# Kernel tuning notes

Measured on AMD Instinct MI355X. Metric: run time of the kernel, lower is better.

Reference implementation:

```python
import jax, jax.numpy as jnp
import numpy as np
from jax.scipy.special import logsumexp

EPS = 0.05        # entropic regularization (blur^p)
N_ITERS = 20      # Sinkhorn iterations
N, M, D = 8192, 8192, 64


def setup_inputs() -> dict:
    key = jax.random.key(0)
    k1, k2, k3, k4 = jax.random.split(key, 4)
    return {
        "a": jax.random.uniform(k1, (N,), dtype=jnp.float32),
        "x": jax.random.normal(k2, (N, D), dtype=jnp.float32),
        "b": jax.random.uniform(k3, (M,), dtype=jnp.float32),
        "y": jax.random.normal(k4, (M, D), dtype=jnp.float32),
    }


def reference(a, x, b, y):
    eps = EPS
    # _normalize_weights: probability simplex
    a = a / jnp.sum(a)
    b = b / jnp.sum(b)
    loga = jnp.log(a)
    logb = jnp.log(b)
    # squared-Euclidean cost C_ij = ||x_i - y_j||^2, built via one GEMM (online kernel's math)
    x2 = jnp.sum(x * x, axis=1)            # [N]
    y2 = jnp.sum(y * y, axis=1)            # [M]
    C = x2[:, None] + y2[None, :] - 2.0 * (x @ y.T)   # [N, M]

    # log-domain Sinkhorn: f_i = -eps * LSE_j( log b_j + (g_j - C_ij)/eps )
    def softmin_rows(g_, C_, logw):   # reduce over columns j -> [N]
        return -eps * logsumexp(logw[None, :] + (g_[None, :] - C_) / eps, axis=1)

    def softmin_cols(f_, C_, logw):   # reduce over rows i -> [M]
        return -eps * logsumexp(logw[:, None] + (f_[:, None] - C_) / eps, axis=0)

    def body(i, fg):
        f_, g_ = fg
        f_ = softmin_rows(g_, C, logb)
        g_ = softmin_cols(f_, C, loga)
        return (f_, g_)

    f0 = jnp.zeros_like(a)
    g0 = jnp.zeros_like(b)
    f, g = jax.lax.fori_loop(0, N_ITERS, body, (f0, g0))

    # GeomLoss-style: one final symmetric update from detached potentials (Danskin)
    f_d = jax.lax.stop_gradient(f)
    g_d = jax.lax.stop_gradient(g)
    f_fin = softmin_rows(g_d, C, logb)
    g_fin = softmin_cols(f_d, C, loga)
    # OT_eps(a, b) = <a, f> + <b, g>
    return jnp.sum(a * f_fin) + jnp.sum(b * g_fin)
```

## Files before the change

### kernel.cpp

```cpp
#include <hip/hip_runtime.h>
#include <hip/hip_bf16.h>

#define EPS       0.05f
#define N_ITERS   20
#define NR        8192
#define DIM       64
#define LOG2E     1.4426950408889634f
#define LN2       0.6931471805599453f
#define S2        (2.0f * LOG2E / EPS)
#define EPSLN2    (EPS * LN2)
#define NEGINF    (-1e30f)

typedef __attribute__((ext_vector_type(8))) short short8;
typedef __attribute__((ext_vector_type(4))) float float4v;

__device__ __forceinline__ float wave_reduce_sum(float v) {
    #pragma unroll
    for (int m = 1; m < 64; m <<= 1) v += __shfl_xor(v, m, 64);
    return v;
}

__device__ __forceinline__ float merge_l(float m0, float s0, float m1, float s1) {
    float M = fmaxf(m0, m1);
    float S = s0 * __builtin_amdgcn_exp2f(m0 - M) + s1 * __builtin_amdgcn_exp2f(m1 - M);
    return M + __builtin_amdgcn_logf(S);
}

__global__ void sums_kernel(const float* __restrict__ a, const float* __restrict__ b,
                            float* __restrict__ sums) {
    __shared__ float red[32];
    int tid = threadIdx.x;
    float pa = 0.f, pb = 0.f;
    for (int i = tid; i < NR; i += blockDim.x) { pa += a[i]; pb += b[i]; }
    pa = wave_reduce_sum(pa);
    pb = wave_reduce_sum(pb);
    int wid = tid >> 6, ln = tid & 63;
    if (ln == 0) { red[wid] = pa; red[wid + 16] = pb; }
    __syncthreads();
    if (tid == 0) {
        float sa = 0.f, sb = 0.f;
        int nw = blockDim.x >> 6;
        for (int w = 0; w < nw; w++) { sa += red[w]; sb += red[w + 16]; }
        sums[0] = logf(sa); sums[1] = logf(sb); sums[2] = sa; sums[3] = sb;
    }
}

__global__ void prep_kernel(const float* __restrict__ x, const float* __restrict__ y,
                            const float* __restrict__ a, const float* __restrict__ b,
                            const float* __restrict__ sums,
                            short8* __restrict__ xr, short8* __restrict__ yr,
                            short8* __restrict__ xs, short8* __restrict__ ys,
                            float* __restrict__ x2, float* __restrict__ y2,
                            float* __restrict__ la2, float* __restrict__ lb2,
                            float2* __restrict__ Pb) {
    int gid = blockIdx.x * 256 + threadIdx.x;
    bool isx = gid < NR * 8;
    int cid = isx ? gid : gid - NR * 8;
    int row = cid >> 3;
    int c   = cid & 7;
    const float4* src = (const float4*)(isx ? x : y);
    float4 v0 = src[row * 16 + c * 2];
    float4 v1 = src[row * 16 + c * 2 + 1];

    short8 st;
    st[0] = __bfloat16_as_short(__float2bfloat16(v0.x));
    st[1] = __bfloat16_as_short(__float2bfloat16(v0.y));
    st[2] = __bfloat16_as_short(__float2bfloat16(v0.z));
    st[3] = __bfloat16_as_short(__float2bfloat16(v0.w));
    st[4] = __bfloat16_as_short(__float2bfloat16(v1.x));
    st[5] = __bfloat16_as_short(__float2bfloat16(v1.y));
    st[6] = __bfloat16_as_short(__float2bfloat16(v1.z));
    st[7] = __bfloat16_as_short(__float2bfloat16(v1.w));

    (isx ? xr : yr)[row * 8 + c] = st;
    int T = row >> 4, ln = row & 15, f = c >> 2, q = c & 3;
    (isx ? xs : ys)[T * 128 + f * 64 + q * 16 + ln] = st;

    float sq = v0.x*v0.x + v0.y*v0.y + v0.z*v0.z + v0.w*v0.w
             + v1.x*v1.x + v1.y*v1.y + v1.z*v1.z + v1.w*v1.w;
    #pragma unroll
    for (int m = 1; m < 8; m <<= 1) sq += __shfl_xor(sq, m, 64);

    if (c == 0) {
        if (isx) {
            x2[row] = sq;
            la2[row] = (logf(a[row]) - sums[0]) * LOG2E;
        } else {
            y2[row] = sq;
            lb2[row] = (logf(b[row]) - sums[1]) * LOG2E;
            Pb[row]      = make_float2(sq * (LOG2E / EPS), 1.0f);
            Pb[NR + row] = make_float2(NEGINF, 0.0f);
        }
    }
}

#define LSE4(acc, c4, mm, ss)                                            \
    {                                                                    \
        float z0 = fmaf(S2, (acc)[0], (c4).x);                           \
        float z1 = fmaf(S2, (acc)[1], (c4).y);                           \
        float z2 = fmaf(S2, (acc)[2], (c4).z);                           \
        float z3 = fmaf(S2, (acc)[3], (c4).w);                           \
        float zm = fmaxf(fmaxf(z0, z1), fmaxf(z2, z3));                  \
        float mn = fmaxf((mm), zm);                                      \
        float e  = __builtin_amdgcn_exp2f((mm) - mn);                    \
        float p  = (__builtin_amdgcn_exp2f(z0 - mn)                      \
                  + __builtin_amdgcn_exp2f(z1 - mn))                     \
                 + (__builtin_amdgcn_exp2f(z2 - mn)                      \
                  + __builtin_amdgcn_exp2f(z3 - mn));                    \
        (ss) = fmaf((ss), e, p);                                         \
        (mm) = mn;                                                       \
    }

__global__ __launch_bounds__(1024, 4) void pass_kernel(
        const short8* __restrict__ matXr,
        const short8* __restrict__ matYs,
        const float2* __restrict__ Pin,
        const float* __restrict__ lw2col,
        float2* __restrict__ Pout) {
    __shared__ __attribute__((aligned(16))) float cbl[4096];
    __shared__ float2 comb[64][16];

    const int tid = threadIdx.x;
    const int bi  = blockIdx.x;
    const int h   = bi & 1;
    const int rb  = (bi >> 1) * 64;
    const int cb0 = h * 4096;

    {
        int j = cb0 + tid * 4;
        const float4* P0 = (const float4*)(Pin + j);
        const float4* P1 = (const float4*)(Pin + NR + j);
        float4 q0 = P0[0], q1 = P0[1];
        float4 r0 = P1[0], r1 = P1[1];
        float4 lw = *(const float4*)(lw2col + j);
        float4 cb;
        cb.x = lw.x - merge_l(q0.x, q0.y, r0.x, r0.y);
        cb.y = lw.y - merge_l(q0.z, q0.w, r0.z, r0.w);
        cb.z = lw.z - merge_l(q1.x, q1.y, r1.x, r1.y);
        cb.w = lw.w - merge_l(q1.z, q1.w, r1.z, r1.w);
        *(float4*)(cbl + tid * 4) = cb;
    }

    const int w    = tid >> 6;
    const int lane = tid & 63;
    const int quad = lane >> 4;
    const int ln   = lane & 15;

    short8 xf0[4], xf1[4];
    #pragma unroll
    for (int t = 0; t < 4; t++) {
        xf0[t] = matXr[(rb + t * 16 + ln) * 8 + quad];
        xf1[t] = matXr[(rb + t * 16 + ln) * 8 + quad + 4];
    }

    const int T0 = h * 256 + w * 16;
    const short8* yp = matYs + (size_t)T0 * 128 + lane;

    float m[4], s[4];
    #pragma unroll
    for (int t = 0; t < 4; t++) { m[t] = NEGINF; s[t] = 0.f; }

    __syncthreads();

    #pragma unroll 2
    for (int jt = 0; jt < 16; jt++) {
        short8 ya0 = yp[0];
        short8 ya1 = yp[64];
        float4 c4  = *(const float4*)(cbl + (w * 16 + jt) * 16 + quad * 4);
        yp += 128;

        float4v acc[4];
        #pragma unroll
        for (int t = 0; t < 4; t++) {
            float4v z = {0.f, 0.f, 0.f, 0.f};
            z = __builtin_amdgcn_mfma_f32_16x16x32_bf16(ya0, xf0[t], z, 0, 0, 0);
            z = __builtin_amdgcn_mfma_f32_16x16x32_bf16(ya1, xf1[t], z, 0, 0, 0);
            acc[t] = z;
        }
        #pragma unroll
        for (int t = 0; t < 4; t++) LSE4(acc[t], c4, m[t], s[t]);
    }

    #pragma unroll
    for (int mask = 16; mask < 64; mask <<= 1) {
        #pragma unroll
        for (int t = 0; t < 4; t++) {
            float mo = __shfl_xor(m[t], mask, 64);
            float so = __shfl_xor(s[t], mask, 64);
            float M  = fmaxf(m[t], mo);
            s[t] = s[t] * __builtin_amdgcn_exp2f(m[t] - M)
                 + so   * __builtin_amdgcn_exp2f(mo   - M);
            m[t] = M;
        }
    }

    if (lane < 16) {
        #pragma unroll
        for (int t = 0; t < 4; t++)
            comb[t * 16 + ln][w] = make_float2(m[t], s[t]);
    }
    __syncthreads();

    if (tid < 64) {
        float2 c = comb[tid][0];
        float M = c.x, S = c.y;
        #pragma unroll
        for (int cc = 1; cc < 16; cc++) {
            float2 p = comb[tid][cc];
            float Mn = fmaxf(M, p.x);
            S = S * __builtin_amdgcn_exp2f(M - Mn)
              + p.y * __builtin_amdgcn_exp2f(p.x - Mn);
            M = Mn;
        }
        Pout[h * NR + rb + tid] = make_float2(M, S);
    }
}

__global__ void reduce_kernel(const float* __restrict__ a, const float* __restrict__ b,
                              const float* __restrict__ sums,
                              const float* __restrict__ x2, const float* __restrict__ y2,
                              const float2* __restrict__ Pff, const float2* __restrict__ Pgf,
                              float* __restrict__ out) {
    __shared__ float red[32];
    int tid = threadIdx.x;
    float da = 0.f, db = 0.f;
    for (int i = tid; i < NR; i += blockDim.x) {
        float2 f0 = Pff[i], f1 = Pff[NR + i];
        float2 g0 = Pgf[i], g1 = Pgf[NR + i];
        float fv = x2[i] - EPSLN2 * merge_l(f0.x, f0.y, f1.x, f1.y);
        float gv = y2[i] - EPSLN2 * merge_l(g0.x, g0.y, g1.x, g1.y);
        da += a[i] * fv;
        db += b[i] * gv;
    }
    da = wave_reduce_sum(da);
    db = wave_reduce_sum(db);
    int wid = tid >> 6, ln = tid & 63;
    if (ln == 0) { red[wid] = da; red[wid + 16] = db; }
    __syncthreads();
    if (tid == 0) {
        float DA = 0.f, DB = 0.f;
        int nw = blockDim.x >> 6;
        for (int w = 0; w < nw; w++) { DA += red[w]; DB += red[w + 16]; }
        out[0] = DA / sums[2] + DB / sums[3];
    }
}

extern "C" void kernel_launch(void* const* d_in, const int* in_sizes, int n_in,
                              void* d_out, int out_size, void* d_ws, size_t ws_size,
                              hipStream_t stream) {
    const float* a = (const float*)d_in[0];
    const float* x = (const float*)d_in[1];
    const float* b = (const float*)d_in[2];
    const float* y = (const float*)d_in[3];

    char* ws = (char*)d_ws;
    short8* xr = (short8*)ws;
    short8* yr = (short8*)(ws + (1 << 20));
    short8* xs = (short8*)(ws + (2 << 20));
    short8* ys = (short8*)(ws + (3 << 20));
    float* fp  = (float*)(ws + (4 << 20));
    float* x2  = fp;
    float* y2  = fp + NR;
    float* la2 = fp + 2 * NR;
    float* lb2 = fp + 3 * NR;
    float2* P   = (float2*)(fp + 4 * NR);
    float2* Pf  = P;
    float2* Pb  = P + 2 * NR;
    float2* Pff = P + 4 * NR;
    float2* Pgf = P + 6 * NR;
    float* sums = (float*)(P + 8 * NR);

    sums_kernel<<<1, 1024, 0, stream>>>(a, b, sums);
    prep_kernel<<<(2 * NR * 8) / 256, 256, 0, stream>>>(x, y, a, b, sums,
                                                        xr, yr, xs, ys,
                                                        x2, y2, la2, lb2, Pb);

    for (int it = 0; it < N_ITERS; it++) {
        pass_kernel<<<256, 1024, 0, stream>>>(xr, ys, Pb, lb2, Pf);
        pass_kernel<<<256, 1024, 0, stream>>>(yr, xs, Pf, la2, Pb);
    }
    pass_kernel<<<256, 1024, 0, stream>>>(xr, ys, Pb, lb2, Pff);
    pass_kernel<<<256, 1024, 0, stream>>>(yr, xs, Pf, la2, Pgf);

    reduce_kernel<<<1, 1024, 0, stream>>>(a, b, sums, x2, y2, Pff, Pgf, (float*)d_out);
}
```

Before: 924.4 us.

## Split columns into four partitions with 128-row blocks per workgroup

Each pass block now covers 128 rows and a quarter of the columns, instead of 64 rows and half the columns. Two groups of eight waves share each 16-column strip, so the Y fragments and column constants are reused across twice as many rows. Each block reads and writes four partial log-sum-exp buffers instead of two, so the consumer merges four partials. Grid size stays at 256 blocks. The price is a larger partial-merge step in each pass and in the final reduction.

```diff
diff --git a/kernel.cpp b/kernel.cpp
--- a/kernel.cpp
+++ b/kernel.cpp
@@ -10,6 +10,7 @@
 #define S2        (2.0f * LOG2E / EPS)
 #define EPSLN2    (EPS * LN2)
 #define NEGINF    (-1e30f)
+#define NSPLIT    4
 
 typedef __attribute__((ext_vector_type(8))) short short8;
 typedef __attribute__((ext_vector_type(4))) float float4v;
@@ -20,9 +21,12 @@
     return v;
 }
 
-__device__ __forceinline__ float merge_l(float m0, float s0, float m1, float s1) {
-    float M = fmaxf(m0, m1);
-    float S = s0 * __builtin_amdgcn_exp2f(m0 - M) + s1 * __builtin_amdgcn_exp2f(m1 - M);
+__device__ __forceinline__ float merge4_l(float2 p0, float2 p1, float2 p2, float2 p3) {
+    float M = fmaxf(fmaxf(p0.x, p1.x), fmaxf(p2.x, p3.x));
+    float S = p0.y * __builtin_amdgcn_exp2f(p0.x - M)
+            + p1.y * __builtin_amdgcn_exp2f(p1.x - M)
+            + p2.y * __builtin_amdgcn_exp2f(p2.x - M)
+            + p3.y * __builtin_amdgcn_exp2f(p3.x - M);
     return M + __builtin_amdgcn_logf(S);
 }
 
@@ -88,8 +92,10 @@
         } else {
             y2[row] = sq;
             lb2[row] = (logf(b[row]) - sums[1]) * LOG2E;
-            Pb[row]      = make_float2(sq * (LOG2E / EPS), 1.0f);
-            Pb[NR + row] = make_float2(NEGINF, 0.0f);
+            Pb[row] = make_float2(sq * (LOG2E / EPS), 1.0f);
+            #pragma unroll
+            for (int k = 1; k < NSPLIT; k++)
+                Pb[k * NR + row] = make_float2(NEGINF, 0.0f);
         }
     }
 }
@@ -117,44 +123,48 @@
         const float2* __restrict__ Pin,
         const float* __restrict__ lw2col,
         float2* __restrict__ Pout) {
-    __shared__ __attribute__((aligned(16))) float cbl[4096];
-    __shared__ float2 comb[64][16];
+    __shared__ __attribute__((aligned(16))) float cbl[2048];
+    __shared__ float2 comb[128][9];
 
     const int tid = threadIdx.x;
     const int bi  = blockIdx.x;
-    const int h   = bi & 1;
-    const int rb  = (bi >> 1) * 64;
-    const int cb0 = h * 4096;
+    const int q4  = bi & 3;
+    const int rb  = (bi >> 2) * 128;
+    const int cb0 = q4 * 2048;
 
     {
-        int j = cb0 + tid * 4;
-        const float4* P0 = (const float4*)(Pin + j);
-        const float4* P1 = (const float4*)(Pin + NR + j);
-        float4 q0 = P0[0], q1 = P0[1];
-        float4 r0 = P1[0], r1 = P1[1];
-        float4 lw = *(const float4*)(lw2col + j);
-        float4 cb;
-        cb.x = lw.x - merge_l(q0.x, q0.y, r0.x, r0.y);
-        cb.y = lw.y - merge_l(q0.z, q0.w, r0.z, r0.w);
-        cb.z = lw.z - merge_l(q1.x, q1.y, r1.x, r1.y);
-        cb.w = lw.w - merge_l(q1.z, q1.w, r1.z, r1.w);
-        *(float4*)(cbl + tid * 4) = cb;
-    }
-
-    const int w    = tid >> 6;
-    const int lane = tid & 63;
-    const int quad = lane >> 4;
-    const int ln   = lane & 15;
+        int j = cb0 + tid * 2;
+        float4 p0 = *(const float4*)(Pin + 0 * NR + j);
+        float4 p1 = *(const float4*)(Pin + 1 * NR + j);
+        float4 p2 = *(const float4*)(Pin + 2 * NR + j);
+        float4 p3 = *(const float4*)(Pin + 3 * NR + j);
+        float2 lw = *(const float2*)(lw2col + j);
+        float2 cb;
+        cb.x = lw.x - merge4_l(make_float2(p0.x, p0.y), make_float2(p1.x, p1.y),
+                               make_float2(p2.x, p2.y), make_float2(p3.x, p3.y));
+        cb.y = lw.y - merge4_l(make_float2(p0.z, p0.w), make_float2(p1.z, p1.w),
+                               make_float2(p2.z, p2.w), make_float2(p3.z, p3.w));
+        *(float2*)(cbl + tid * 2) = cb;
+    }
+
+    const int w     = tid >> 6;
+    const int lane  = tid & 63;
+    const int quad  = lane >> 4;
+    const int ln    = lane & 15;
+    const int strip = w & 7;
+    const int rh    = w >> 3;
 
     short8 xf0[4], xf1[4];
     #pragma unroll
     for (int t = 0; t < 4; t++) {
-        xf0[t] = matXr[(rb + t * 16 + ln) * 8 + quad];
-        xf1[t] = matXr[(rb + t * 16 + ln) * 8 + quad + 4];
-    }
-
-    const int T0 = h * 256 + w * 16;
+        int r = rb + rh * 64 + t * 16 + ln;
+        xf0[t] = matXr[r * 8 + quad];
+        xf1[t] = matXr[r * 8 + quad + 4];
+    }
+
+    const int T0 = q4 * 128 + strip * 16;
     const short8* yp = matYs + (size_t)T0 * 128 + lane;
+    const float* cbs = cbl + strip * 256 + quad * 4;
 
     float m[4], s[4];
     #pragma unroll
@@ -166,7 +176,7 @@
     for (int jt = 0; jt < 16; jt++) {
         short8 ya0 = yp[0];
         short8 ya1 = yp[64];
-        float4 c4  = *(const float4*)(cbl + (w * 16 + jt) * 16 + quad * 4);
+        float4 c4  = *(const float4*)(cbs + jt * 16);
         yp += 128;
 
         float4v acc[4];
@@ -197,22 +207,22 @@
     if (lane < 16) {
         #pragma unroll
         for (int t = 0; t < 4; t++)
-            comb[t * 16 + ln][w] = make_float2(m[t], s[t]);
-    }
-    __syncthreads();
-
-    if (tid < 64) {
+            comb[rh * 64 + t * 16 + ln][strip] = make_float2(m[t], s[t]);
+    }
+    __syncthreads();
+
+    if (tid < 128) {
         float2 c = comb[tid][0];
         float M = c.x, S = c.y;
         #pragma unroll
-        for (int cc = 1; cc < 16; cc++) {
+        for (int cc = 1; cc < 8; cc++) {
             float2 p = comb[tid][cc];
             float Mn = fmaxf(M, p.x);
             S = S * __builtin_amdgcn_exp2f(M - Mn)
               + p.y * __builtin_amdgcn_exp2f(p.x - Mn);
             M = Mn;
         }
-        Pout[h * NR + rb + tid] = make_float2(M, S);
+        Pout[q4 * NR + rb + tid] = make_float2(M, S);
     }
 }
 
@@ -225,10 +235,10 @@
     int tid = threadIdx.x;
     float da = 0.f, db = 0.f;
     for (int i = tid; i < NR; i += blockDim.x) {
-        float2 f0 = Pff[i], f1 = Pff[NR + i];
-        float2 g0 = Pgf[i], g1 = Pgf[NR + i];
-        float fv = x2[i] - EPSLN2 * merge_l(f0.x, f0.y, f1.x, f1.y);
-        float gv = y2[i] - EPSLN2 * merge_l(g0.x, g0.y, g1.x, g1.y);
+        float fv = x2[i] - EPSLN2 * merge4_l(Pff[i], Pff[NR + i],
+                                             Pff[2 * NR + i], Pff[3 * NR + i]);
+        float gv = y2[i] - EPSLN2 * merge4_l(Pgf[i], Pgf[NR + i],
+                                             Pgf[2 * NR + i], Pgf[3 * NR + i]);
         da += a[i] * fv;
         db += b[i] * gv;
     }
@@ -265,10 +275,10 @@
     float* lb2 = fp + 3 * NR;
     float2* P   = (float2*)(fp + 4 * NR);
     float2* Pf  = P;
-    float2* Pb  = P + 2 * NR;
-    float2* Pff = P + 4 * NR;
-    float2* Pgf = P + 6 * NR;
-    float* sums = (float*)(P + 8 * NR);
+    float2* Pb  = P + NSPLIT * NR;
+    float2* Pff = P + 2 * NSPLIT * NR;
+    float2* Pgf = P + 3 * NSPLIT * NR;
+    float* sums = (float*)(P + 4 * NSPLIT * NR);
 
     sums_kernel<<<1, 1024, 0, stream>>>(a, b, sums);
     prep_kernel<<<(2 * NR * 8) / 256, 256, 0, stream>>>(x, y, a, b, sums,
```

Measured after the change: 944.2 us. 1.02x slower.
